# Optimization experiments

Measured on AMD Instinct MI355X. Metric: run time of the kernel, lower is better.

Reference implementation:

```python
import jax, jax.numpy as jnp
import numpy as np

WS = 7
SHIFT = 3
NH = 6


def _rel_index(ws):
    coords = np.stack(np.meshgrid(np.arange(ws), np.arange(ws), indexing='ij'))  # (2, ws, ws)
    cf = coords.reshape(2, -1)                       # (2, N)
    rel = (cf[:, :, None] - cf[:, None, :]).transpose(1, 2, 0).copy()  # (N, N, 2)
    rel[:, :, 0] += ws - 1
    rel[:, :, 1] += ws - 1
    rel[:, :, 0] *= 2 * ws - 1
    return rel.sum(-1)                               # (N, N) int


def _attn_mask(Hp, Wp, ws, shift):
    img = np.zeros((Hp, Wp))
    cnt = 0
    sl = (slice(0, -ws), slice(-ws, -shift), slice(-shift, None))
    for h in sl:
        for w in sl:
            img[h, w] = cnt
            cnt += 1
    mw = img.reshape(Hp // ws, ws, Wp // ws, ws).transpose(0, 2, 1, 3).reshape(-1, ws * ws)
    am = mw[:, None, :] - mw[:, :, None]
    return np.where(am != 0, -100.0, 0.0).astype(np.float32)  # (num_win, N, N)


def _ln(x, g, b, eps=1e-5):
    m = x.mean(-1, keepdims=True)
    v = ((x - m) ** 2).mean(-1, keepdims=True)
    return (x - m) * jax.lax.rsqrt(v + eps) * g + b


def _forward(x, qkv_w, qkv_b, proj_w, proj_b, rpb_table,
             norm1_g, norm1_b, norm2_g, norm2_b,
             mlp_w1, mlp_b1, mlp_w2, mlp_b2, H, W):
    B, L, C = x.shape
    ws, nh = WS, NH
    hd = C // nh
    N = ws * ws
    shortcut = x

    h = _ln(x, norm1_g, norm1_b).reshape(B, H, W, C)
    pad_b = (ws - H % ws) % ws
    pad_r = (ws - W % ws) % ws
    if pad_b or pad_r:
        h = jnp.pad(h, ((0, 0), (0, pad_b), (0, pad_r), (0, 0)))
    Hp, Wp = H + pad_b, W + pad_r
    shift = SHIFT if min(Hp, Wp) > ws else 0
    if shift:
        h = jnp.roll(h, (-shift, -shift), axis=(1, 2))

    nwh, nww = Hp // ws, Wp // ws
    # window partition -> (B*num_win, N, C)
    win = h.reshape(B, nwh, ws, nww, ws, C).transpose(0, 1, 3, 2, 4, 5).reshape(-1, N, C)

    qkv = (win @ qkv_w.T + qkv_b).reshape(-1, N, 3, nh, hd).transpose(2, 0, 3, 1, 4)
    q, k, v = qkv[0], qkv[1], qkv[2]          # (BW, nh, N, hd)
    attn = jnp.einsum('bhnd,bhmd->bhnm', q, k) * (hd ** -0.5)

    ridx = _rel_index(ws)
    bias = rpb_table[ridx.reshape(-1)].reshape(N, N, nh).transpose(2, 0, 1)  # (nh, N, N)
    attn = attn + bias[None]

    if shift:
        m = jnp.asarray(_attn_mask(Hp, Wp, ws, shift))  # (num_win, N, N)
        nw = nwh * nww
        attn = attn.reshape(B, nw, nh, N, N) + m[None, :, None]
        attn = attn.reshape(-1, nh, N, N)

    attn = jax.nn.softmax(attn, axis=-1)
    out = jnp.einsum('bhnm,bhmd->bnhd', attn, v).reshape(-1, N, C)
    out = out @ proj_w.T + proj_b

    # window reverse -> (B, Hp, Wp, C)
    out = out.reshape(B, nwh, nww, ws, ws, C).transpose(0, 1, 3, 2, 4, 5).reshape(B, Hp, Wp, C)
    if shift:
        out = jnp.roll(out, (shift, shift), axis=(1, 2))
    out = out[:, :H, :W].reshape(B, H * W, C)

    x = shortcut + out
    h2 = _ln(x, norm2_g, norm2_b)
    h2 = jax.nn.gelu(h2 @ mlp_w1.T + mlp_b1, approximate=False) @ mlp_w2.T + mlp_b2
    return x + h2


def setup_inputs() -> dict:
    key = jax.random.key(0)
    ks = jax.random.split(key, 8)
    B, H, W, C = 32, 56, 56, 192
    hid = 4 * C
    s = 0.02
    return {
        'x': jax.random.normal(ks[0], (B, H * W, C), jnp.float32),
        'qkv_w': jax.random.normal(ks[1], (3 * C, C), jnp.float32) * s,
        'qkv_b': jnp.zeros((3 * C,), jnp.float32),
        'proj_w': jax.random.normal(ks[2], (C, C), jnp.float32) * s,
        'proj_b': jnp.zeros((C,), jnp.float32),
        'rpb_table': jax.random.normal(ks[3], ((2 * WS - 1) ** 2, NH), jnp.float32) * s,
        'norm1_g': jnp.ones((C,), jnp.float32),
        'norm1_b': jnp.zeros((C,), jnp.float32),
        'norm2_g': jnp.ones((C,), jnp.float32),
        'norm2_b': jnp.zeros((C,), jnp.float32),
        'mlp_w1': jax.random.normal(ks[4], (hid, C), jnp.float32) * s,
        'mlp_b1': jnp.zeros((hid,), jnp.float32),
        'mlp_w2': jax.random.normal(ks[5], (C, hid), jnp.float32) * s,
        'mlp_b2': jnp.zeros((C,), jnp.float32),
        'H': H,
        'W': W,
    }


def reference(x, qkv_w, qkv_b, proj_w, proj_b, rpb_table,
              norm1_g, norm1_b, norm2_g, norm2_b,
              mlp_w1, mlp_b1, mlp_w2, mlp_b2, H, W):
    return _forward(x, qkv_w, qkv_b, proj_w, proj_b, rpb_table,
                    norm1_g, norm1_b, norm2_g, norm2_b,
                    mlp_w1, mlp_b1, mlp_w2, mlp_b2, int(H), int(W))
```

## Files before the change

### kernel.cpp

```cpp
#include <hip/hip_runtime.h>
#include <hip/hip_bf16.h>
#include <math.h>

typedef short short8 __attribute__((ext_vector_type(8)));
typedef float floatx4 __attribute__((ext_vector_type(4)));

__device__ __forceinline__ void async16(const void* g, void* l) {
  __builtin_amdgcn_global_load_lds((const __attribute__((address_space(1))) void*)g,
                                   (__attribute__((address_space(3))) void*)l, 16, 0, 0);
}

__global__ void cvt_kernel(const float* __restrict__ in, __hip_bfloat16* __restrict__ o, int n) {
  int i = blockIdx.x * 256 + threadIdx.x;
  if (i < n) o[i] = __float2bfloat16(in[i]);
}

__global__ void table_kernel(const float* __restrict__ rpb, float* __restrict__ tb) {
  int i = blockIdx.x * 256 + threadIdx.x;
  if (i >= 4 * 6 * 64 * 64) return;
  int n = i & 63, m = (i >> 6) & 63;
  int hc = i >> 12, head = hc % 6, cls = hc / 6;
  float v;
  if (m >= 49 || n >= 49) {
    v = -30000.0f;
  } else {
    int rm = m / 7, cm = m - rm * 7;
    int rn = n / 7, cn = n - rn * 7;
    float bias = rpb[((rm - rn + 6) * 13 + (cm - cn + 6)) * 6 + head];
    int regm = ((cls & 2) ? (rm < 4 ? 1 : 2) : 0) * 3 + ((cls & 1) ? (cm < 4 ? 1 : 2) : 0);
    int regn = ((cls & 2) ? (rn < 4 ? 1 : 2) : 0) * 3 + ((cls & 1) ? (cn < 4 ? 1 : 2) : 0);
    v = bias + (regm != regn ? -100.0f : 0.0f);
  }
  tb[i] = v;
}

template<bool WINDOWED>
__global__ __launch_bounds__(256) void ln_kernel(const float* __restrict__ x,
                                                 const float* __restrict__ g,
                                                 const float* __restrict__ b,
                                                 __hip_bfloat16* __restrict__ out) {
  int w = threadIdx.x >> 6, lane = threadIdx.x & 63;
  int row = blockIdx.x * 4 + w;
  size_t src_row;
  if (WINDOWED) {
    int wi = row / 49, t = row - wi * 49;
    int bb = wi >> 6, wim = wi & 63, wh = wim >> 3, wwn = wim & 7;
    int r = t / 7, c = t - r * 7;
    int y = wh * 7 + r + 3;  if (y >= 56) y -= 56;
    int xp = wwn * 7 + c + 3; if (xp >= 56) xp -= 56;
    src_row = (size_t)bb * 3136 + (size_t)y * 56 + xp;
  } else {
    src_row = row;
  }
  const float* src = x + src_row * 192;
  float v0 = src[lane], v1 = src[lane + 64], v2 = src[lane + 128];
  float s = v0 + v1 + v2;
#pragma unroll
  for (int off = 32; off > 0; off >>= 1) s += __shfl_xor(s, off, 64);
  float mean = s * (1.0f / 192.0f);
  float d0 = v0 - mean, d1 = v1 - mean, d2 = v2 - mean;
  float q = d0 * d0 + d1 * d1 + d2 * d2;
#pragma unroll
  for (int off = 32; off > 0; off >>= 1) q += __shfl_xor(q, off, 64);
  float rstd = rsqrtf(q * (1.0f / 192.0f) + 1e-5f);
  __hip_bfloat16* o = out + (size_t)row * 192;
  o[lane]       = __float2bfloat16(d0 * rstd * g[lane]       + b[lane]);
  o[lane + 64]  = __float2bfloat16(d1 * rstd * g[lane + 64]  + b[lane + 64]);
  o[lane + 128] = __float2bfloat16(d2 * rstd * g[lane + 128] + b[lane + 128]);
}

template<int K, int EPI>
__global__ __launch_bounds__(256) void gemm_bt(const __hip_bfloat16* __restrict__ A,
                                               const __hip_bfloat16* __restrict__ B,
                                               const float* __restrict__ bias,
                                               const float* residF,
                                               float* outF,
                                               __hip_bfloat16* __restrict__ outB,
                                               int N) {
  __shared__ __hip_bfloat16 sA[128 * 64];
  __shared__ __hip_bfloat16 sB[64 * 64];
  const int m0 = blockIdx.y * 128;
  const int n0 = blockIdx.x * 64;
  const int tid = threadIdx.x;
  const int w = tid >> 6, lane = tid & 63;
  const int quad = lane >> 4, l16 = lane & 15;
  const int wr = w >> 1, wc = w & 1;

  floatx4 acc[4][2] = {};

  const __hip_bfloat16* Abase = A + (size_t)m0 * K;
  const __hip_bfloat16* Bbase = B + (size_t)n0 * K;

  for (int k0 = 0; k0 < K; k0 += 64) {
    const __hip_bfloat16* Ag = Abase + k0;
#pragma unroll
    for (int it = 0; it < 4; ++it) {
      int cb = ((it * 4 + w) << 6);
      int c = cb + lane;
      async16(Ag + (size_t)(c >> 3) * K + ((c & 7) << 3), &sA[cb * 8]);
    }
    const __hip_bfloat16* Bg = Bbase + k0;
#pragma unroll
    for (int it = 0; it < 2; ++it) {
      int cb = ((it * 4 + w) << 6);
      int c = cb + lane;
      async16(Bg + (size_t)(c >> 3) * K + ((c & 7) << 3), &sB[cb * 8]);
    }
    __syncthreads();

#pragma unroll
    for (int kk = 0; kk < 64; kk += 32) {
      short8 af[4], bf[2];
#pragma unroll
      for (int ri = 0; ri < 4; ++ri)
        af[ri] = *(const short8*)&sA[(wr * 64 + ri * 16 + l16) * 64 + kk + quad * 8];
#pragma unroll
      for (int ci = 0; ci < 2; ++ci)
        bf[ci] = *(const short8*)&sB[(wc * 32 + ci * 16 + l16) * 64 + kk + quad * 8];
#pragma unroll
      for (int ri = 0; ri < 4; ++ri)
#pragma unroll
        for (int ci = 0; ci < 2; ++ci)
          acc[ri][ci] = __builtin_amdgcn_mfma_f32_16x16x32_bf16(af[ri], bf[ci], acc[ri][ci], 0, 0, 0);
    }
    __syncthreads();
  }

  const int m_base = m0 + wr * 64;
#pragma unroll
  for (int ri = 0; ri < 4; ++ri) {
#pragma unroll
    for (int ci = 0; ci < 2; ++ci) {
      const int ccol = n0 + wc * 32 + ci * 16 + l16;
      const float bv = bias[ccol];
#pragma unroll
      for (int reg = 0; reg < 4; ++reg) {
        const int row = m_base + ri * 16 + quad * 4 + reg;
        float v = acc[ri][ci][reg] + bv;
        if (EPI == 0) {
          outB[(size_t)row * N + ccol] = __float2bfloat16(v);
        } else {
          int wi = row / 49, t = row - wi * 49;
          int bb = wi >> 6, wim = wi & 63, wh = wim >> 3, wwn = wim & 7;
          int r = t / 7, c = t - r * 7;
          int y = wh * 7 + r + 3;  if (y >= 56) y -= 56;
          int xp = wwn * 7 + c + 3; if (xp >= 56) xp -= 56;
          size_t drow = ((size_t)bb * 3136 + (size_t)y * 56 + xp) * 192 + ccol;
          outF[drow] = v + residF[drow];
        }
      }
    }
  }
}

__global__ __launch_bounds__(256, 3) void mlp_kernel(const __hip_bfloat16* __restrict__ A,
                                                     const __hip_bfloat16* __restrict__ W1,
                                                     const float* __restrict__ b1,
                                                     const __hip_bfloat16* __restrict__ W2,
                                                     const float* __restrict__ b2,
                                                     float* __restrict__ out) {
  __shared__ __hip_bfloat16 sW1[32 * 192];
  __shared__ __hip_bfloat16 sW2[192 * 32];
  __shared__ __hip_bfloat16 sH[64 * 40];
  const int tid = threadIdx.x;
  const int w = tid >> 6, lane = tid & 63;
  const int quad = lane >> 4, l16 = lane & 15;
  const int wr = w >> 1, wc = w & 1;
  const size_t rowblk = (size_t)blockIdx.x * 64;

  short8 af[6];
  {
    const __hip_bfloat16* arow = A + (rowblk + w * 16 + l16) * 192 + quad * 8;
#pragma unroll
    for (int j = 0; j < 6; ++j) af[j] = *(const short8*)(arow + 32 * j);
  }

  floatx4 acc[2][6] = {};

  for (int hb = 0; hb < 768; hb += 32) {
    __syncthreads();
    {
      const char* s1 = (const char*)(W1 + hb * 192);
#pragma unroll
      for (int it = 0; it < 3; ++it) {
        int c = it * 256 + tid;
        async16(s1 + c * 16, (char*)sW1 + c * 16);
      }
      const char* s2 = (const char*)W2 + hb * 2;
#pragma unroll
      for (int it = 0; it < 3; ++it) {
        int c = it * 256 + tid;
        async16(s2 + (size_t)(c >> 2) * 1536 + (c & 3) * 16, (char*)sW2 + c * 16);
      }
    }
    __syncthreads();

    floatx4 hc[2] = {};
#pragma unroll
    for (int j = 0; j < 6; ++j) {
#pragma unroll
      for (int t = 0; t < 2; ++t) {
        short8 bw = *(const short8*)&sW1[(t * 16 + l16) * 192 + j * 32 + quad * 8];
        hc[t] = __builtin_amdgcn_mfma_f32_16x16x32_bf16(af[j], bw, hc[t], 0, 0, 0);
      }
    }
#pragma unroll
    for (int t = 0; t < 2; ++t) {
      const float bv = b1[hb + t * 16 + l16];
#pragma unroll
      for (int r = 0; r < 4; ++r) {
        float v = hc[t][r] + bv;
        float g = 0.5f * v * (1.0f + erff(v * 0.70710678118654752f));
        sH[(w * 16 + quad * 4 + r) * 40 + t * 16 + l16] = __float2bfloat16(g);
      }
    }
    __syncthreads();

    short8 ah[2], bw2[6];
#pragma unroll
    for (int mi = 0; mi < 2; ++mi)
      ah[mi] = *(const short8*)&sH[(wr * 32 + mi * 16 + l16) * 40 + quad * 8];
#pragma unroll
    for (int ni = 0; ni < 6; ++ni)
      bw2[ni] = *(const short8*)&sW2[(wc * 96 + ni * 16 + l16) * 32 + quad * 8];
#pragma unroll
    for (int mi = 0; mi < 2; ++mi)
#pragma unroll
      for (int ni = 0; ni < 6; ++ni)
        acc[mi][ni] = __builtin_amdgcn_mfma_f32_16x16x32_bf16(ah[mi], bw2[ni], acc[mi][ni], 0, 0, 0);
  }

#pragma unroll
  for (int mi = 0; mi < 2; ++mi) {
#pragma unroll
    for (int ni = 0; ni < 6; ++ni) {
      const int ccol = wc * 96 + ni * 16 + l16;
      const float bv = b2[ccol];
#pragma unroll
      for (int r = 0; r < 4; ++r) {
        const size_t row = rowblk + wr * 32 + mi * 16 + quad * 4 + r;
        float* p = out + row * 192 + ccol;
        *p = *p + acc[mi][ni][r] + bv;
      }
    }
  }
}

__global__ __launch_bounds__(256) void attn_kernel(const __hip_bfloat16* __restrict__ qkv,
                                                   const float* __restrict__ table,
                                                   __hip_bfloat16* __restrict__ out) {
  __shared__ __hip_bfloat16 Plds[4][64 * 72];
  __shared__ __hip_bfloat16 Vt[4][32 * 64];
  const int slot = threadIdx.x >> 6, lane = threadIdx.x & 63;
  const int quad = lane >> 4, l16 = lane & 15;

  const int wg = blockIdx.x * 4 + slot;
  const int wi = wg / 6, head = wg - wi * 6;
  const int wim = wi & 63, wh = wim >> 3, wwn = wim & 7;
  const int cls = ((wh == 7) ? 2 : 0) + ((wwn == 7) ? 1 : 0);
  const __hip_bfloat16* base = qkv + (size_t)wi * 49 * 576 + head * 32;

  const __hip_bfloat16* vbase = base + 384;
#pragma unroll
  for (int it = 0; it < 4; ++it) {
    int p = it * 64 + lane;
    if (p < 196) {
      int k = p >> 2, c = p & 3;
      short8 sv = *(const short8*)(vbase + k * 576 + c * 8);
#pragma unroll
      for (int j = 0; j < 8; ++j)
        Vt[slot][(c * 8 + j) * 64 + k] = ((const __hip_bfloat16*)&sv)[j];
    }
  }
#pragma unroll
  for (int it = 0; it < 8; ++it) {
    int p = it * 64 + lane;
    if (p < 480) {
      int k = 49 + (p >> 5), n = p & 31;
      Vt[slot][n * 64 + k] = __float2bfloat16(0.0f);
    }
  }

  short8 aq[4], bk[4];
#pragma unroll
  for (int t = 0; t < 4; ++t) {
    int m = l16 + 16 * t; if (m > 48) m = 48;
    aq[t] = *(const short8*)(base + m * 576 + quad * 8);
    bk[t] = *(const short8*)(base + 192 + m * 576 + quad * 8);
  }

  floatx4 sc[4][4] = {};
#pragma unroll
  for (int ti = 0; ti < 4; ++ti)
#pragma unroll
    for (int tj = 0; tj < 4; ++tj)
      sc[ti][tj] = __builtin_amdgcn_mfma_f32_16x16x32_bf16(aq[ti], bk[tj], sc[ti][tj], 0, 0, 0);

  const float scale = 0.17677669529663689f;
  const float* tb = table + (((size_t)cls * 6 + head) << 12);
  float linv[4][4];
#pragma unroll
  for (int ti = 0; ti < 4; ++ti) {
#pragma unroll
    for (int r = 0; r < 4; ++r) {
      const int row = 16 * ti + quad * 4 + r;
      const float* trow = tb + row * 64 + l16;
      float v0 = sc[ti][0][r] * scale + trow[0];
      float v1 = sc[ti][1][r] * scale + trow[16];
      float v2 = sc[ti][2][r] * scale + trow[32];
      float v3 = sc[ti][3][r] * scale + trow[48];
      float mx = fmaxf(fmaxf(v0, v1), fmaxf(v2, v3));
      mx = fmaxf(mx, __shfl_xor(mx, 1));
      mx = fmaxf(mx, __shfl_xor(mx, 2));
      mx = fmaxf(mx, __shfl_xor(mx, 4));
      mx = fmaxf(mx, __shfl_xor(mx, 8));
      v0 = __expf(v0 - mx); v1 = __expf(v1 - mx);
      v2 = __expf(v2 - mx); v3 = __expf(v3 - mx);
      float sm = (v0 + v1) + (v2 + v3);
      sm += __shfl_xor(sm, 1);
      sm += __shfl_xor(sm, 2);
      sm += __shfl_xor(sm, 4);
      sm += __shfl_xor(sm, 8);
      linv[ti][r] = 1.0f / sm;
      __hip_bfloat16* pr = &Plds[slot][row * 72 + l16];
      pr[0]  = __float2bfloat16(v0);
      pr[16] = __float2bfloat16(v1);
      pr[32] = __float2bfloat16(v2);
      pr[48] = __float2bfloat16(v3);
    }
  }
  __syncthreads();

  floatx4 oc[4][2] = {};
#pragma unroll
  for (int kb = 0; kb < 64; kb += 32) {
    short8 ap[4], bv[2];
#pragma unroll
    for (int ti = 0; ti < 4; ++ti)
      ap[ti] = *(const short8*)&Plds[slot][(l16 + 16 * ti) * 72 + kb + quad * 8];
#pragma unroll
    for (int t2 = 0; t2 < 2; ++t2)
      bv[t2] = *(const short8*)&Vt[slot][(l16 + 16 * t2) * 64 + kb + quad * 8];
#pragma unroll
    for (int ti = 0; ti < 4; ++ti)
#pragma unroll
      for (int t2 = 0; t2 < 2; ++t2)
        oc[ti][t2] = __builtin_amdgcn_mfma_f32_16x16x32_bf16(ap[ti], bv[t2], oc[ti][t2], 0, 0, 0);
  }

#pragma unroll
  for (int ti = 0; ti < 4; ++ti) {
#pragma unroll
    for (int reg = 0; reg < 4; ++reg) {
      const int row = 16 * ti + quad * 4 + reg;
      if (row < 49) {
        __hip_bfloat16* op = out + ((size_t)wi * 49 + row) * 192 + head * 32 + l16;
        const float li = linv[ti][reg];
        op[0]  = __float2bfloat16(oc[ti][0][reg] * li);
        op[16] = __float2bfloat16(oc[ti][1][reg] * li);
      }
    }
  }
}

extern "C" void kernel_launch(void* const* d_in, const int* in_sizes, int n_in,
                              void* d_out, int out_size, void* d_ws, size_t ws_size,
                              hipStream_t stream) {
  const float* x      = (const float*)d_in[0];
  const float* qkv_w  = (const float*)d_in[1];
  const float* qkv_b  = (const float*)d_in[2];
  const float* proj_w = (const float*)d_in[3];
  const float* proj_b = (const float*)d_in[4];
  const float* rpb    = (const float*)d_in[5];
  const float* n1g    = (const float*)d_in[6];
  const float* n1b    = (const float*)d_in[7];
  const float* n2g    = (const float*)d_in[8];
  const float* n2b    = (const float*)d_in[9];
  const float* w1     = (const float*)d_in[10];
  const float* b1     = (const float*)d_in[11];
  const float* w2     = (const float*)d_in[12];
  const float* b2     = (const float*)d_in[13];
  float* out = (float*)d_out;

  char* ws = (char*)d_ws;
  __hip_bfloat16* bufB = (__hip_bfloat16*)ws;
  __hip_bfloat16* bufA = (__hip_bfloat16*)(ws + 115605504);
  __hip_bfloat16* wqb = (__hip_bfloat16*)(ws + 115605504 + 38535168);
  __hip_bfloat16* wpb = wqb + 110592;
  __hip_bfloat16* w1b = wpb + 36864;
  __hip_bfloat16* w2b = w1b + 147456;
  float* tablef = (float*)(ws + 115605504 + 38535168 + 884736);

  cvt_kernel<<<(110592 + 255) / 256, 256, 0, stream>>>(qkv_w, wqb, 110592);
  cvt_kernel<<<(36864  + 255) / 256, 256, 0, stream>>>(proj_w, wpb, 36864);
  cvt_kernel<<<(147456 + 255) / 256, 256, 0, stream>>>(w1, w1b, 147456);
  cvt_kernel<<<(147456 + 255) / 256, 256, 0, stream>>>(w2, w2b, 147456);
  table_kernel<<<384, 256, 0, stream>>>(rpb, tablef);

  ln_kernel<true><<<25088, 256, 0, stream>>>(x, n1g, n1b, bufA);
  gemm_bt<192, 0><<<dim3(9, 784), 256, 0, stream>>>(bufA, wqb, qkv_b, nullptr, nullptr, bufB, 576);
  attn_kernel<<<3072, 256, 0, stream>>>(bufB, tablef, bufA);
  gemm_bt<192, 1><<<dim3(3, 784), 256, 0, stream>>>(bufA, wpb, proj_b, x, out, nullptr, 192);
  ln_kernel<false><<<25088, 256, 0, stream>>>(out, n2g, n2b, bufA);
  mlp_kernel<<<1568, 256, 0, stream>>>(bufA, w1b, b1, w2b, b2, out);
}
```

Measured before the change: 522.8 us.

## Swizzle LDS tiles in GEMMs and double-buffer W1 in MLP kernel

Applies an XOR swizzle to the LDS layout of the A and B tiles in the projection GEMM and of W1 in the MLP kernel, to avoid bank conflicts when the 16-byte MFMA fragments are read. In the MLP kernel, W1 tiles are double-buffered so the next tile's async load overlaps the current compute, which removes one barrier per iteration. W2 fragments are now read directly from global memory into registers instead of being staged through LDS. The trade-off is more LDS for the second W1 buffer and uncoalesced, strided global reads of W2 that depend on cache hits.

```diff
diff --git a/kernel.cpp b/kernel.cpp
--- a/kernel.cpp
+++ b/kernel.cpp
@@ -97,14 +97,16 @@
     for (int it = 0; it < 4; ++it) {
       int cb = ((it * 4 + w) << 6);
       int c = cb + lane;
-      async16(Ag + (size_t)(c >> 3) * K + ((c & 7) << 3), &sA[cb * 8]);
+      int jsrc = (c & 7) ^ ((c >> 3) & 7);
+      async16(Ag + (size_t)(c >> 3) * K + (jsrc << 3), &sA[cb * 8]);
     }
     const __hip_bfloat16* Bg = Bbase + k0;
 #pragma unroll
     for (int it = 0; it < 2; ++it) {
       int cb = ((it * 4 + w) << 6);
       int c = cb + lane;
-      async16(Bg + (size_t)(c >> 3) * K + ((c & 7) << 3), &sB[cb * 8]);
+      int jsrc = (c & 7) ^ ((c >> 3) & 7);
+      async16(Bg + (size_t)(c >> 3) * K + (jsrc << 3), &sB[cb * 8]);
     }
     __syncthreads();
 
@@ -112,11 +114,17 @@
     for (int kk = 0; kk < 64; kk += 32) {
       short8 af[4], bf[2];
 #pragma unroll
-      for (int ri = 0; ri < 4; ++ri)
-        af[ri] = *(const short8*)&sA[(wr * 64 + ri * 16 + l16) * 64 + kk + quad * 8];
-#pragma unroll
-      for (int ci = 0; ci < 2; ++ci)
-        bf[ci] = *(const short8*)&sB[(wc * 32 + ci * 16 + l16) * 64 + kk + quad * 8];
+      for (int ri = 0; ri < 4; ++ri) {
+        int rA = wr * 64 + ri * 16 + l16;
+        int slot = ((kk >> 3) + quad) ^ (rA & 7);
+        af[ri] = *(const short8*)&sA[rA * 64 + (slot << 3)];
+      }
+#pragma unroll
+      for (int ci = 0; ci < 2; ++ci) {
+        int rB = wc * 32 + ci * 16 + l16;
+        int slot = ((kk >> 3) + quad) ^ (rB & 7);
+        bf[ci] = *(const short8*)&sB[rB * 64 + (slot << 3)];
+      }
 #pragma unroll
       for (int ri = 0; ri < 4; ++ri)
 #pragma unroll
@@ -159,8 +167,7 @@
                                                      const __hip_bfloat16* __restrict__ W2,
                                                      const float* __restrict__ b2,
                                                      float* __restrict__ out) {
-  __shared__ __hip_bfloat16 sW1[32 * 192];
-  __shared__ __hip_bfloat16 sW2[192 * 32];
+  __shared__ __hip_bfloat16 sW1[2 * 32 * 192];
   __shared__ __hip_bfloat16 sH[64 * 40];
   const int tid = threadIdx.x;
   const int w = tid >> 6, lane = tid & 63;
@@ -177,30 +184,35 @@
 
   floatx4 acc[2][6] = {};
 
-  for (int hb = 0; hb < 768; hb += 32) {
+#pragma unroll
+  for (int it = 0; it < 3; ++it) {
+    int c = it * 256 + tid;
+    int row = c / 24, jj = c - row * 24;
+    int jsrc = jj ^ (row & 7);
+    async16(W1 + row * 192 + (jsrc << 3), &sW1[(c & ~63) * 8]);
+  }
+
+  for (int i = 0; i < 24; ++i) {
+    const int hb = i * 32;
+    __hip_bfloat16* cw = sW1 + (i & 1) * (32 * 192);
     __syncthreads();
+
+    short8 bw2[6];
     {
-      const char* s1 = (const char*)(W1 + hb * 192);
-#pragma unroll
-      for (int it = 0; it < 3; ++it) {
-        int c = it * 256 + tid;
-        async16(s1 + c * 16, (char*)sW1 + c * 16);
-      }
-      const char* s2 = (const char*)W2 + hb * 2;
-#pragma unroll
-      for (int it = 0; it < 3; ++it) {
-        int c = it * 256 + tid;
-        async16(s2 + (size_t)(c >> 2) * 1536 + (c & 3) * 16, (char*)sW2 + c * 16);
-      }
-    }
-    __syncthreads();
+      const __hip_bfloat16* w2p = W2 + hb + quad * 8;
+#pragma unroll
+      for (int ni = 0; ni < 6; ++ni)
+        bw2[ni] = *(const short8*)(w2p + (size_t)(wc * 96 + ni * 16 + l16) * 768);
+    }
 
     floatx4 hc[2] = {};
 #pragma unroll
     for (int j = 0; j < 6; ++j) {
 #pragma unroll
       for (int t = 0; t < 2; ++t) {
-        short8 bw = *(const short8*)&sW1[(t * 16 + l16) * 192 + j * 32 + quad * 8];
+        int r = t * 16 + l16;
+        int slot = (j * 4 + quad) ^ (r & 7);
+        short8 bw = *(const short8*)&cw[r * 192 + (slot << 3)];
         hc[t] = __builtin_amdgcn_mfma_f32_16x16x32_bf16(af[j], bw, hc[t], 0, 0, 0);
       }
     }
@@ -216,13 +228,22 @@
     }
     __syncthreads();
 
-    short8 ah[2], bw2[6];
+    if (i < 23) {
+      const __hip_bfloat16* W1n = W1 + (hb + 32) * 192;
+      __hip_bfloat16* nw = sW1 + ((i + 1) & 1) * (32 * 192);
+#pragma unroll
+      for (int it = 0; it < 3; ++it) {
+        int c = it * 256 + tid;
+        int row = c / 24, jj = c - row * 24;
+        int jsrc = jj ^ (row & 7);
+        async16(W1n + row * 192 + (jsrc << 3), &nw[(c & ~63) * 8]);
+      }
+    }
+
+    short8 ah[2];
 #pragma unroll
     for (int mi = 0; mi < 2; ++mi)
       ah[mi] = *(const short8*)&sH[(wr * 32 + mi * 16 + l16) * 40 + quad * 8];
-#pragma unroll
-    for (int ni = 0; ni < 6; ++ni)
-      bw2[ni] = *(const short8*)&sW2[(wc * 96 + ni * 16 + l16) * 32 + quad * 8];
 #pragma unroll
     for (int mi = 0; mi < 2; ++mi)
 #pragma unroll
```

After: 549.0 us. +5.0%, slower.
